# Optimization experiments

Measured on AMD Instinct MI355X. Metric: run time of the kernel, lower is better.

## Reference

```python
import jax, jax.numpy as jnp
import numpy as np

B, T, H, O = 256, 512, 1024, 10


def setup_inputs() -> dict:
    key = jax.random.key(0)
    ks = jax.random.split(key, 6)
    return {
        "x": jax.random.normal(ks[0], (B, T), dtype=jnp.float32),
        "W_hx": jax.random.normal(ks[1], (1, H), dtype=jnp.float32),
        "W_hh": jax.random.normal(ks[2], (H, H), dtype=jnp.float32),
        "W_ph": jax.random.normal(ks[3], (H, O), dtype=jnp.float32),
        "b_h": jax.random.normal(ks[4], (H,), dtype=jnp.float32),
        "b_o": jax.random.normal(ks[5], (O,), dtype=jnp.float32),
    }


def reference(x, W_hx, W_hh, W_ph, b_h, b_o):
    # Precompute input projections for all steps at once: [B,T,1]@[1,H] -> [B,T,H]
    xp = x[:, :, None] * W_hx[None, None, 0, :] + b_h  # [B,T,H]
    h0 = jnp.zeros((x.shape[0], W_hh.shape[0]), dtype=x.dtype)

    def step(h, xp_t):
        h = jnp.tanh(xp_t + h @ W_hh)
        return h, None

    h_final, _ = jax.lax.scan(step, h0, jnp.swapaxes(xp, 0, 1))  # scan over T
    return h_final @ W_ph + b_o
```

## Files before the change

### kernel.cpp

```cpp
#include <hip/hip_runtime.h>
#include <math.h>


#define HH 1024
#define TT 512
#define BB 256
#define OO 10
#define NG 16
#define NCT 16
#define NTH 256
#define KH 512

__device__ __forceinline__ float tanh_ref(float x) {
    const float kClamp = 7.99881172180175781f;
    float xc = fminf(fmaxf(x, -kClamp), kClamp);
    float x2 = __fmul_rn(xc, xc);
    float p = -2.76076847742355e-16f;
    p = fmaf(x2, p,  2.00018790482477e-13f);
    p = fmaf(x2, p, -8.60467152213735e-11f);
    p = fmaf(x2, p,  5.12229709037114e-08f);
    p = fmaf(x2, p,  1.48572235717979e-05f);
    p = fmaf(x2, p,  6.37261928875436e-04f);
    p = fmaf(x2, p,  4.89352455891786e-03f);
    p = __fmul_rn(xc, p);
    float q = 1.19825839466702e-06f;
    q = fmaf(x2, q, 1.18534705686654e-04f);
    q = fmaf(x2, q, 2.26843463243900e-03f);
    q = fmaf(x2, q, 4.89352518554385e-03f);
    float r = __fdiv_rn(p, q);
    return (fabsf(x) < 0.0004f) ? x : r;
}

#define MACC(acc, hv, wv) acc = __fadd_rn(acc, __fmul_rn(hv, wv))

#define GROUPSYNC_FAST(target_) {                                                   \
    __syncthreads();                              \
    if (tid == 0) {                                                                  \
        __hip_atomic_fetch_add(&ctr[g], 1, __ATOMIC_RELAXED, __HIP_MEMORY_SCOPE_AGENT); \
        while (__hip_atomic_load(&ctr[g], __ATOMIC_RELAXED, __HIP_MEMORY_SCOPE_AGENT)   \
               < (target_))                                                          \
            __builtin_amdgcn_s_sleep(2);                                             \
    }                                                                                \
    __syncthreads();                                                                 \
    asm volatile("buffer_inv" ::: "memory");        \
}

__global__ void __launch_bounds__(NTH, 1) rnn_persist(
    const float* __restrict__ x, const float* __restrict__ Whx,
    const float* __restrict__ Whh, const float* __restrict__ Wph,
    const float* __restrict__ bh, const float* __restrict__ bo,
    float* __restrict__ out, float* __restrict__ ws)
{
    __shared__ float wlds[KH][64];

    const int bid  = blockIdx.x;
    const int ct   = (bid >> 3) & 15;
    const int g    = ((bid & 7) << 1) | (bid >> 7);
    const int tid  = threadIdx.x;
    const int w    = tid >> 6;
    const int lane = tid & 63;
    const int j0   = ct * 64;
    const int j    = j0 + lane;
    const int r0w  = g * 16 + w * 4;

    float* hAbuf = ws;
    float* hBbuf = ws + (BB * HH);
    int*   ctr   = (int*)(ws + 2 * BB * HH);

    const float whx_j = Whx[j];
    const float bh_j  = bh[j];

    #pragma unroll
    for (int i = 0; i < 32; ++i) {
        const int s = tid + i * NTH;
        const int k = s >> 4;
        const int c = s & 15;
        ((float4*)wlds)[s] = ((const float4*)(Whh + (size_t)k * HH + j0))[c];
    }

    #pragma unroll
    for (int r = 0; r < 4; ++r)
        hAbuf[(size_t)(r0w + r) * HH + j] = 0.0f;
    GROUPSYNC_FAST(NCT)

    for (int t = 0; t < TT; ++t) {
        const float* hsrc = (t & 1) ? hBbuf : hAbuf;
        float*       hdst = (t & 1) ? hAbuf : hBbuf;

        const float* h0p = hsrc + (size_t)(r0w + 0) * HH;
        const float* h1p = hsrc + (size_t)(r0w + 1) * HH;
        const float* h2p = hsrc + (size_t)(r0w + 2) * HH;
        const float* h3p = hsrc + (size_t)(r0w + 3) * HH;
        const float* wp1 = Whh + (size_t)KH * HH + j;

        float a0 = 0.f, a1 = 0.f, a2 = 0.f, a3 = 0.f;
        float b0 = 0.f, b1 = 0.f, b2 = 0.f, b3 = 0.f;

        #pragma unroll 2
        for (int k4 = 0; k4 < KH; k4 += 4) {
            const float4 ha0 = *(const float4*)(h0p + k4);
            const float4 ha1 = *(const float4*)(h1p + k4);
            const float4 ha2 = *(const float4*)(h2p + k4);
            const float4 ha3 = *(const float4*)(h3p + k4);
            const float4 hb0 = *(const float4*)(h0p + KH + k4);
            const float4 hb1 = *(const float4*)(h1p + KH + k4);
            const float4 hb2 = *(const float4*)(h2p + KH + k4);
            const float4 hb3 = *(const float4*)(h3p + KH + k4);
            const float w0 = wlds[k4 + 0][lane];
            const float w1 = wlds[k4 + 1][lane];
            const float w2 = wlds[k4 + 2][lane];
            const float w3 = wlds[k4 + 3][lane];
            const float v0 = wp1[0];
            const float v1 = wp1[HH];
            const float v2 = wp1[2 * HH];
            const float v3 = wp1[3 * HH];
            wp1 += 4 * HH;
            MACC(a0, ha0.x, w0); MACC(a1, ha1.x, w0); MACC(a2, ha2.x, w0); MACC(a3, ha3.x, w0);
            MACC(b0, hb0.x, v0); MACC(b1, hb1.x, v0); MACC(b2, hb2.x, v0); MACC(b3, hb3.x, v0);
            MACC(a0, ha0.y, w1); MACC(a1, ha1.y, w1); MACC(a2, ha2.y, w1); MACC(a3, ha3.y, w1);
            MACC(b0, hb0.y, v1); MACC(b1, hb1.y, v1); MACC(b2, hb2.y, v1); MACC(b3, hb3.y, v1);
            MACC(a0, ha0.z, w2); MACC(a1, ha1.z, w2); MACC(a2, ha2.z, w2); MACC(a3, ha3.z, w2);
            MACC(b0, hb0.z, v2); MACC(b1, hb1.z, v2); MACC(b2, hb2.z, v2); MACC(b3, hb3.z, v2);
            MACC(a0, ha0.w, w3); MACC(a1, ha1.w, w3); MACC(a2, ha2.w, w3); MACC(a3, ha3.w, w3);
            MACC(b0, hb0.w, v3); MACC(b1, hb1.w, v3); MACC(b2, hb2.w, v3); MACC(b3, hb3.w, v3);
        }

        {
            const float m0 = __fadd_rn(a0, b0);
            const float m1 = __fadd_rn(a1, b1);
            const float m2 = __fadd_rn(a2, b2);
            const float m3 = __fadd_rn(a3, b3);
            const float xv0 = x[(r0w + 0) * TT + t];
            const float xv1 = x[(r0w + 1) * TT + t];
            const float xv2 = x[(r0w + 2) * TT + t];
            const float xv3 = x[(r0w + 3) * TT + t];
            hdst[(size_t)(r0w + 0) * HH + j] =
                tanh_ref(__fadd_rn(__fadd_rn(__fmul_rn(xv0, whx_j), bh_j), m0));
            hdst[(size_t)(r0w + 1) * HH + j] =
                tanh_ref(__fadd_rn(__fadd_rn(__fmul_rn(xv1, whx_j), bh_j), m1));
            hdst[(size_t)(r0w + 2) * HH + j] =
                tanh_ref(__fadd_rn(__fadd_rn(__fmul_rn(xv2, whx_j), bh_j), m2));
            hdst[(size_t)(r0w + 3) * HH + j] =
                tanh_ref(__fadd_rn(__fadd_rn(__fmul_rn(xv3, whx_j), bh_j), m3));
        }

        GROUPSYNC_FAST(NCT * (t + 2))
    }

    if (ct == 0) {
        #pragma unroll 1
        for (int r = 0; r < 4; ++r) {
            const int row = r0w + r;
            #pragma unroll 1
            for (int o = 0; o < OO; ++o) {
                float v = 0.0f;
                #pragma unroll
                for (int m = 0; m < HH / 64; ++m) {
                    const int k = lane + (m << 6);
                    v = fmaf(hAbuf[(size_t)row * HH + k], Wph[k * OO + o], v);
                }
                #pragma unroll
                for (int s = 32; s > 0; s >>= 1) v += __shfl_down(v, s, 64);
                if (lane == 0) out[row * OO + o] = v + bo[o];
            }
        }
    }
}

extern "C" void kernel_launch(void* const* d_in, const int* in_sizes, int n_in,
                              void* d_out, int out_size, void* d_ws, size_t ws_size,
                              hipStream_t stream) {
    const float* x   = (const float*)d_in[0];
    const float* Whx = (const float*)d_in[1];
    const float* Whh = (const float*)d_in[2];
    const float* Wph = (const float*)d_in[3];
    const float* bh  = (const float*)d_in[4];
    const float* bo  = (const float*)d_in[5];
    float* out = (float*)d_out;
    float* ws  = (float*)d_ws;

    hipMemsetAsync((char*)d_ws + (size_t)2 * BB * HH * 4, 0, NG * sizeof(int), stream);

    void* args[] = {(void*)&x, (void*)&Whx, (void*)&Whh, (void*)&Wph,
                    (void*)&bh, (void*)&bo, (void*)&out, (void*)&ws};
    hipLaunchCooperativeKernel((void*)rnn_persist, dim3(NG * NCT), dim3(NTH),
                               args, 0, stream);
}
```

Before: 18.61 ms.

## Retile to 8 batch groups × 32 column tiles with full W_hh slice in LDS

Changes the block decomposition from 16 batch groups of 16 rows × 16 column tiles of 64 to 8 groups of 32 rows × 32 tiles of 32 columns. Each block now keeps its entire 1024×32 W_hh slice in shared memory, so the second half of K no longer streams from global memory every timestep. The output projection loop is reworked so four waves share all 32 rows. In exchange, each group barrier now involves 32 blocks instead of 16, and half-wave lanes read the same LDS column, which may cause broadcasts or bank conflicts.

```diff
diff --git a/kernel.cpp b/kernel.cpp
--- a/kernel.cpp
+++ b/kernel.cpp
@@ -6,8 +6,8 @@
 #define TT 512
 #define BB 256
 #define OO 10
-#define NG 16
-#define NCT 16
+#define NGRP 8
+#define NCT 32
 #define NTH 256
 #define KH 512
 
@@ -34,7 +34,7 @@
 #define MACC(acc, hv, wv) acc = __fadd_rn(acc, __fmul_rn(hv, wv))
 
 #define GROUPSYNC_FAST(target_) {                                                   \
-    __syncthreads();                              \
+    __syncthreads();                                                                 \
     if (tid == 0) {                                                                  \
         __hip_atomic_fetch_add(&ctr[g], 1, __ATOMIC_RELAXED, __HIP_MEMORY_SCOPE_AGENT); \
         while (__hip_atomic_load(&ctr[g], __ATOMIC_RELAXED, __HIP_MEMORY_SCOPE_AGENT)   \
@@ -42,7 +42,7 @@
             __builtin_amdgcn_s_sleep(2);                                             \
     }                                                                                \
     __syncthreads();                                                                 \
-    asm volatile("buffer_inv" ::: "memory");        \
+    asm volatile("buffer_inv" ::: "memory");                                         \
 }
 
 __global__ void __launch_bounds__(NTH, 1) rnn_persist(
@@ -51,17 +51,19 @@
     const float* __restrict__ bh, const float* __restrict__ bo,
     float* __restrict__ out, float* __restrict__ ws)
 {
-    __shared__ float wlds[KH][64];
+    __shared__ float wlds[HH][32];
 
     const int bid  = blockIdx.x;
-    const int ct   = (bid >> 3) & 15;
-    const int g    = ((bid & 7) << 1) | (bid >> 7);
+    const int g    = bid & 7;
+    const int ct   = bid >> 3;
     const int tid  = threadIdx.x;
     const int w    = tid >> 6;
     const int lane = tid & 63;
-    const int j0   = ct * 64;
-    const int j    = j0 + lane;
-    const int r0w  = g * 16 + w * 4;
+    const int c32  = lane & 31;
+    const int slot = lane >> 5;
+    const int j0   = ct * 32;
+    const int j    = j0 + c32;
+    const int r0w  = g * 32 + w * 8 + slot * 4;
 
     float* hAbuf = ws;
     float* hBbuf = ws + (BB * HH);
@@ -73,9 +75,9 @@
     #pragma unroll
     for (int i = 0; i < 32; ++i) {
         const int s = tid + i * NTH;
-        const int k = s >> 4;
-        const int c = s & 15;
-        ((float4*)wlds)[s] = ((const float4*)(Whh + (size_t)k * HH + j0))[c];
+        const int k = s >> 3;
+        const int c4 = s & 7;
+        ((float4*)wlds)[s] = ((const float4*)(Whh + (size_t)k * HH + j0))[c4];
     }
 
     #pragma unroll
@@ -91,7 +93,6 @@
         const float* h1p = hsrc + (size_t)(r0w + 1) * HH;
         const float* h2p = hsrc + (size_t)(r0w + 2) * HH;
         const float* h3p = hsrc + (size_t)(r0w + 3) * HH;
-        const float* wp1 = Whh + (size_t)KH * HH + j;
 
         float a0 = 0.f, a1 = 0.f, a2 = 0.f, a3 = 0.f;
         float b0 = 0.f, b1 = 0.f, b2 = 0.f, b3 = 0.f;
@@ -106,15 +107,14 @@
             const float4 hb1 = *(const float4*)(h1p + KH + k4);
             const float4 hb2 = *(const float4*)(h2p + KH + k4);
             const float4 hb3 = *(const float4*)(h3p + KH + k4);
-            const float w0 = wlds[k4 + 0][lane];
-            const float w1 = wlds[k4 + 1][lane];
-            const float w2 = wlds[k4 + 2][lane];
-            const float w3 = wlds[k4 + 3][lane];
-            const float v0 = wp1[0];
-            const float v1 = wp1[HH];
-            const float v2 = wp1[2 * HH];
-            const float v3 = wp1[3 * HH];
-            wp1 += 4 * HH;
+            const float w0 = wlds[k4 + 0][c32];
+            const float w1 = wlds[k4 + 1][c32];
+            const float w2 = wlds[k4 + 2][c32];
+            const float w3 = wlds[k4 + 3][c32];
+            const float v0 = wlds[KH + k4 + 0][c32];
+            const float v1 = wlds[KH + k4 + 1][c32];
+            const float v2 = wlds[KH + k4 + 2][c32];
+            const float v3 = wlds[KH + k4 + 3][c32];
             MACC(a0, ha0.x, w0); MACC(a1, ha1.x, w0); MACC(a2, ha2.x, w0); MACC(a3, ha3.x, w0);
             MACC(b0, hb0.x, v0); MACC(b1, hb1.x, v0); MACC(b2, hb2.x, v0); MACC(b3, hb3.x, v0);
             MACC(a0, ha0.y, w1); MACC(a1, ha1.y, w1); MACC(a2, ha2.y, w1); MACC(a3, ha3.y, w1);
@@ -149,20 +149,18 @@
 
     if (ct == 0) {
         #pragma unroll 1
-        for (int r = 0; r < 4; ++r) {
-            const int row = r0w + r;
-            #pragma unroll 1
-            for (int o = 0; o < OO; ++o) {
-                float v = 0.0f;
-                #pragma unroll
-                for (int m = 0; m < HH / 64; ++m) {
-                    const int k = lane + (m << 6);
-                    v = fmaf(hAbuf[(size_t)row * HH + k], Wph[k * OO + o], v);
-                }
-                #pragma unroll
-                for (int s = 32; s > 0; s >>= 1) v += __shfl_down(v, s, 64);
-                if (lane == 0) out[row * OO + o] = v + bo[o];
+        for (int p = w; p < 32 * OO; p += 4) {
+            const int rr = p / OO, o = p % OO;
+            const int row = g * 32 + rr;
+            float v = 0.0f;
+            #pragma unroll
+            for (int m = 0; m < HH / 64; ++m) {
+                const int k = lane + (m << 6);
+                v = fmaf(hAbuf[(size_t)row * HH + k], Wph[k * OO + o], v);
             }
+            #pragma unroll
+            for (int s = 32; s > 0; s >>= 1) v += __shfl_down(v, s, 64);
+            if (lane == 0) out[row * OO + o] = v + bo[o];
         }
     }
 }
@@ -179,10 +177,10 @@
     float* out = (float*)d_out;
     float* ws  = (float*)d_ws;
 
-    hipMemsetAsync((char*)d_ws + (size_t)2 * BB * HH * 4, 0, NG * sizeof(int), stream);
+    hipMemsetAsync((char*)d_ws + (size_t)2 * BB * HH * 4, 0, 64, stream);
 
     void* args[] = {(void*)&x, (void*)&Whx, (void*)&Whh, (void*)&Wph,
                     (void*)&bh, (void*)&bo, (void*)&out, (void*)&ws};
-    hipLaunchCooperativeKernel((void*)rnn_persist, dim3(NG * NCT), dim3(NTH),
+    hipLaunchCooperativeKernel((void*)rnn_persist, dim3(NGRP * NCT), dim3(NTH),
                                args, 0, stream);
 }
```

New measurement: 20.95 ms. 12.6% more time.
